# Optimization experiments

Hardware: AMD Instinct MI355X
Metric: run time of the kernel (lower is better)

Reference implementation:

```python
import jax, jax.numpy as jnp
import numpy as np

V, E, H, B, S, T, OOV = 50000, 128, 256, 32, 400, 16, 20


def setup_inputs() -> dict:
    key = jax.random.key(0)
    ks = jax.random.split(key, 20)
    def p(i, shape, s=0.02):
        return jax.random.normal(ks[i], shape, dtype=jnp.float32) * s
    z = lambda *shape: jnp.zeros(shape, dtype=jnp.float32)
    return {
        'input_seq': jax.random.randint(ks[0], (B, S), 0, V),
        'input_seq_ext': jax.random.randint(ks[1], (B, S), 0, V + OOV),
        'target_seq': jax.random.randint(ks[2], (B, T), 0, V),
        'embedding': p(3, (V, E)),
        'enc_Wih_f': p(4, (3 * H, E)), 'enc_Whh_f': p(5, (3 * H, H)),
        'enc_bih_f': z(3 * H), 'enc_bhh_f': z(3 * H),
        'enc_Wih_b': p(6, (3 * H, E)), 'enc_Whh_b': p(7, (3 * H, H)),
        'enc_bih_b': z(3 * H), 'enc_bhh_b': z(3 * H),
        'proj_W': p(8, (H, 2 * H)), 'proj_b': z(H),
        'bridge_W': p(9, (H, 2 * H)), 'bridge_b': z(H),
        'dec_Wih': p(10, (3 * H, E + 2 * H)), 'dec_Whh': p(11, (3 * H, H)),
        'dec_bih': z(3 * H), 'dec_bhh': z(3 * H),
        'attn_Wq': p(12, (H, H)), 'attn_We': p(13, (1, H)),
        'lin_W': p(14, (H, E + 3 * H)), 'lin_b': z(H),
        'pgen_W': p(15, (1, E + 3 * H)), 'pgen_b': z(1),
        'out_W': p(16, (V, H)), 'out_b': z(V),
    }


def gru_cell(x, h, Wih, Whh, bih, bhh):
    # PyTorch GRU cell math
    gi = x @ Wih.T + bih
    gh = h @ Whh.T + bhh
    ir, iz, inn = jnp.split(gi, 3, axis=-1)
    hr, hz, hn = jnp.split(gh, 3, axis=-1)
    r = jax.nn.sigmoid(ir + hr)
    zg = jax.nn.sigmoid(iz + hz)
    n = jnp.tanh(inn + r * hn)
    return (1.0 - zg) * n + zg * h


def run_gru(xs, h0, Wih, Whh, bih, bhh):
    def step(h, x):
        h2 = gru_cell(x, h, Wih, Whh, bih, bhh)
        return h2, h2
    hT, hs = jax.lax.scan(step, h0, xs)
    return hs, hT


def reference(input_seq, input_seq_ext, target_seq, embedding,
              enc_Wih_f, enc_Whh_f, enc_bih_f, enc_bhh_f,
              enc_Wih_b, enc_Whh_b, enc_bih_b, enc_bhh_b,
              proj_W, proj_b, bridge_W, bridge_b,
              dec_Wih, dec_Whh, dec_bih, dec_bhh,
              attn_Wq, attn_We, lin_W, lin_b,
              pgen_W, pgen_b, out_W, out_b):
    Bsz, Slen = input_seq.shape
    Tlen = target_seq.shape[1]
    Hd = bridge_W.shape[0]
    dt = embedding.dtype

    # ---- encoder (bidirectional GRU) ----
    emb_src = embedding[input_seq].transpose(1, 0, 2)  # (S,B,E)
    h0e = jnp.zeros((Bsz, Hd), dt)
    hs_f, hf = run_gru(emb_src, h0e, enc_Wih_f, enc_Whh_f, enc_bih_f, enc_bhh_f)
    hs_b_rev, hb = run_gru(emb_src[::-1], h0e, enc_Wih_b, enc_Whh_b, enc_bih_b, enc_bhh_b)
    enc_states = jnp.concatenate([hs_f, hs_b_rev[::-1]], axis=-1)  # (S,B,2H)
    proj = enc_states @ proj_W.T + proj_b                           # (S,B,H)
    h = jnp.tanh(jnp.concatenate([hf, hb], axis=-1) @ bridge_W.T + bridge_b)  # (B,H)

    rows = jnp.arange(Bsz)
    toks = target_seq[:, :Tlen - 1].T  # teacher forcing, (T-1,B)

    def dec_step(h, tok):
        e = embedding[tok]                                            # (B,E)
        scores = jnp.tanh(h @ attn_Wq.T + proj) @ attn_We[0]          # (S,B)
        alphas = jax.nn.softmax(scores, axis=0)                       # softmax over seq dim
        context = jnp.einsum('sb,sbd->bd', alphas, enc_states)        # (B,2H)
        h2 = gru_cell(jnp.concatenate([e, context], axis=-1), h,
                      dec_Wih, dec_Whh, dec_bih, dec_bhh)             # (B,H)
        cat = jnp.concatenate([e, h2, context], axis=-1)              # (B,E+3H)
        p_gen = jax.nn.sigmoid(cat @ pgen_W.T + pgen_b)               # (B,1)
        logits = (cat @ lin_W.T + lin_b) @ out_W.T + out_b            # (B,V)
        gen = p_gen * jax.nn.softmax(logits, axis=-1)
        attn = (1.0 - p_gen) * alphas.T                               # (B,S)
        ext = jnp.concatenate([gen, jnp.zeros((Bsz, OOV), dt)], axis=-1) + 1e-12
        ext = ext.at[rows[:, None], input_seq_ext].add(attn)          # scatter_add copy dist
        return h2, jnp.log(ext)

    _, outs = jax.lax.scan(dec_step, h, toks)                         # (T-1,B,V+OOV)
    out0 = jnp.zeros((1,) + outs.shape[1:], outs.dtype)               # t=0 row stays zero
    return jnp.concatenate([out0, outs], axis=0)                      # (T,B,V+OOV)
```

## Files before the change

### kernel.cpp

```cpp
#include <hip/hip_runtime.h>

#define SLEN 400
#define BATCH 32
#define TLEN 16
#define NDEC 15
#define EDIM 128
#define HDIM 256
#define H3 768
#define VVOC 50000
#define VEXT 50020
#define SCHUNK 50

__device__ __forceinline__ float frcp(float x){ return __builtin_amdgcn_rcpf(x); }
__device__ __forceinline__ float fsig(float x){ return frcp(1.f + __expf(-x)); }
__device__ __forceinline__ float ftanh(float x){
  float e = __expf(2.f*x);
  return 1.f - 2.f*frcp(e + 1.f);
}

typedef _Float16 h2 __attribute__((ext_vector_type(2)));
typedef _Float16 half8 __attribute__((ext_vector_type(8)));
typedef float floatx4 __attribute__((ext_vector_type(4)));

__device__ __forceinline__ h2 u2h(unsigned u){ return __builtin_bit_cast(h2, u); }
__device__ __forceinline__ unsigned pkh(float a, float b){
  h2 v; v.x=(_Float16)a; v.y=(_Float16)b;
  return __builtin_bit_cast(unsigned, v);
}

#if __has_builtin(__builtin_amdgcn_fdot2)
__device__ __forceinline__ float fdot2h(h2 a, h2 b, float c){
  return __builtin_amdgcn_fdot2(a, b, c, false);
}
#else
__device__ __forceinline__ float fdot2h(h2 a, h2 b, float c){
  return fmaf((float)a.x,(float)b.x, fmaf((float)a.y,(float)b.y, c));
}
#endif

__device__ __forceinline__ float wred_sum(float v){
  #pragma unroll
  for (int o=32;o>0;o>>=1) v += __shfl_down(v,o,64);
  return v;
}
__device__ __forceinline__ float wred_max(float v){
  #pragma unroll
  for (int o=32;o>0;o>>=1) v = fmaxf(v, __shfl_down(v,o,64));
  return v;
}
__device__ __forceinline__ float block_max(float v, float* red){
  v = wred_max(v);
  int lane = threadIdx.x & 63, wid = threadIdx.x >> 6;
  if (!lane) red[wid] = v;
  __syncthreads();
  if (threadIdx.x == 0){
    float m = red[0];
    int nw = blockDim.x >> 6;
    for (int w=1;w<nw;++w) m = fmaxf(m, red[w]);
    red[0] = m;
  }
  __syncthreads();
  v = red[0];
  __syncthreads();
  return v;
}
__device__ __forceinline__ float block_sum(float v, float* red){
  v = wred_sum(v);
  int lane = threadIdx.x & 63, wid = threadIdx.x >> 6;
  if (!lane) red[wid] = v;
  __syncthreads();
  if (threadIdx.x == 0){
    float m = red[0];
    int nw = blockDim.x >> 6;
    for (int w=1;w<nw;++w) m += red[w];
    red[0] = m;
  }
  __syncthreads();
  v = red[0];
  __syncthreads();
  return v;
}

__global__ __launch_bounds__(64) void k_embed(
    const int* __restrict__ input_seq, const int* __restrict__ target_seq,
    const float* __restrict__ embedding,
    _Float16* __restrict__ emb16, float* __restrict__ cat_all, _Float16* __restrict__ cat16)
{
  int row = blockIdx.x;
  if (row < SLEN*BATCH) {
    int s = row >> 5, b = row & 31;
    int tok = input_seq[b*SLEN + s];
    float2 v = ((const float2*)(embedding + (size_t)tok*EDIM))[threadIdx.x];
    ((unsigned*)(emb16 + (size_t)row*EDIM))[threadIdx.x] = pkh(v.x, v.y);
  } else {
    int rr = row - SLEN*BATCH;
    int t = rr >> 5, b = rr & 31;
    int tok = target_seq[b*TLEN + t];
    float2 v = ((const float2*)(embedding + (size_t)tok*EDIM))[threadIdx.x];
    ((float2*)(cat_all + (size_t)rr*896))[threadIdx.x] = v;
    ((unsigned*)(cat16 + (size_t)rr*896))[threadIdx.x] = pkh(v.x, v.y);
  }
}

__global__ __launch_bounds__(256) void k_cvtv(
    const float* __restrict__ S, _Float16* __restrict__ D, int n8)
{
  int i = blockIdx.x*256 + threadIdx.x;
  if (i >= n8) return;
  float4 a = ((const float4*)S)[i*2];
  float4 b = ((const float4*)S)[i*2+1];
  uint4 o;
  o.x = pkh(a.x,a.y); o.y = pkh(a.z,a.w);
  o.z = pkh(b.x,b.y); o.w = pkh(b.z,b.w);
  ((uint4*)D)[i] = o;
}

__global__ void k_cvtk(
    const float* __restrict__ W, uint4* __restrict__ D, int ldw, int coloff)
{
  int row = blockIdx.x, k8 = threadIdx.x, nrows = gridDim.x;
  const float* s = W + (size_t)row*ldw + coloff + k8*8;
  float4 x = *(const float4*)s;
  float4 y = *(const float4*)(s+4);
  uint4 o;
  o.x = pkh(x.x,x.y); o.y = pkh(x.z,x.w);
  o.z = pkh(y.x,y.y); o.w = pkh(y.z,y.w);
  D[(size_t)k8*nrows + row] = o;
}

__global__ __launch_bounds__(256) void k_gmm(
    const _Float16* __restrict__ A, int lda,
    const _Float16* __restrict__ W, int ldw,
    const float* __restrict__ bias,
    float* __restrict__ C, _Float16* __restrict__ C16, int ldc,
    int M, int N, int K, int rev)
{
  __shared__ __align__(16) _Float16 Al[128*64];
  __shared__ __align__(16) _Float16 Wl[128*64];
  int tid = threadIdx.x;
  int wv = tid >> 6, l = tid & 63;
  int wr = (wv>>1)*64, wc = (wv&1)*64;
  int lr = l & 15, lh = l >> 4;
  int m0 = blockIdx.y*128, n0 = blockIdx.x*128;
  floatx4 acc[4][4];
  #pragma unroll
  for (int i=0;i<4;++i)
    #pragma unroll
    for (int jn=0;jn<4;++jn) acc[i][jn] = (floatx4){0.f,0.f,0.f,0.f};

  for (int kc=0; kc<K; kc+=64){
    #pragma unroll
    for (int i=0;i<4;++i){
      int idx = tid + i*256;
      int row = idx>>3, c = idx&7;
      int m = m0+row;
      uint4 v = {0u,0u,0u,0u};
      if (m < M){
        int am = m;
        if (rev){ int s = m>>5; am = ((SLEN-1-s)<<5)|(m&31); }
        v = *(const uint4*)&A[(size_t)am*lda + kc + c*8];
      }
      *(uint4*)&Al[row*64 + ((c ^ (row&7))<<3)] = v;
    }
    #pragma unroll
    for (int i=0;i<4;++i){
      int idx = tid + i*256;
      int row = idx>>3, c = idx&7;
      int n = n0+row;
      uint4 v = {0u,0u,0u,0u};
      if (n < N) v = *(const uint4*)&W[(size_t)n*ldw + kc + c*8];
      *(uint4*)&Wl[row*64 + ((c ^ (row&7))<<3)] = v;
    }
    __syncthreads();
    #pragma unroll
    for (int ks=0; ks<2; ++ks){
      half8 af0, af1, af2, af3, bf0, bf1, bf2, bf3;
      {
        int c = ks*4 + lh;
        int r0 = wr + 0*16 + lr, r1 = wr + 1*16 + lr, r2 = wr + 2*16 + lr, r3 = wr + 3*16 + lr;
        af0 = *(const half8*)&Al[r0*64 + ((c ^ (r0&7))<<3)];
        af1 = *(const half8*)&Al[r1*64 + ((c ^ (r1&7))<<3)];
        af2 = *(const half8*)&Al[r2*64 + ((c ^ (r2&7))<<3)];
        af3 = *(const half8*)&Al[r3*64 + ((c ^ (r3&7))<<3)];
        int n0l = wc + 0*16 + lr, n1l = wc + 1*16 + lr, n2l = wc + 2*16 + lr, n3l = wc + 3*16 + lr;
        bf0 = *(const half8*)&Wl[n0l*64 + ((c ^ (n0l&7))<<3)];
        bf1 = *(const half8*)&Wl[n1l*64 + ((c ^ (n1l&7))<<3)];
        bf2 = *(const half8*)&Wl[n2l*64 + ((c ^ (n2l&7))<<3)];
        bf3 = *(const half8*)&Wl[n3l*64 + ((c ^ (n3l&7))<<3)];
      }
      half8 afs[4] = {af0, af1, af2, af3};
      half8 bfs[4] = {bf0, bf1, bf2, bf3};
      #pragma unroll
      for (int mi=0;mi<4;++mi)
        #pragma unroll
        for (int ni=0;ni<4;++ni)
          acc[mi][ni] = __builtin_amdgcn_mfma_f32_16x16x32_f16(afs[mi], bfs[ni], acc[mi][ni], 0,0,0);
    }
    __syncthreads();
  }
  #pragma unroll
  for (int mi=0;mi<4;++mi){
    #pragma unroll
    for (int q=0;q<4;++q){
      int m = m0 + wr + mi*16 + lh*4 + q;
      if (m < M){
        #pragma unroll
        for (int ni=0;ni<4;++ni){
          int n = n0 + wc + ni*16 + lr;
          if (n < N){
            float v = acc[mi][ni][q] + bias[n];
            if (C)   C[(size_t)m*ldc + n] = v;
            if (C16) C16[(size_t)m*ldc + n] = (_Float16)v;
          }
        }
      }
    }
  }
}

#define L20(M) M(12) M(13) M(14) M(15) M(16) M(17) M(18) M(19) M(20) M(21) \
               M(22) M(23) M(24) M(25) M(26) M(27) M(28) M(29) M(30) M(31)

__global__ __launch_bounds__(768) void k_enc(
    const float* __restrict__ gi_f, const float* __restrict__ gi_b,
    const uint4* __restrict__ W16_f, const uint4* __restrict__ W16_b,
    const float* __restrict__ bhh_f, const float* __restrict__ bhh_b,
    float* __restrict__ enc_states)
{
  int dir = blockIdx.x >> 5, b = blockIdx.x & 31;
  int jj = threadIdx.x;
  const float* gi  = dir ? gi_b  : gi_f;
  const uint4* Wp  = (dir ? W16_b : W16_f) + jj;
  float bh = (dir ? bhh_b : bhh_f)[jj];

  __shared__ __align__(16) unsigned hpk[HDIM/2];
  __shared__ __align__(16) float st[H3];
  __shared__ uint4 Wlds[12][H3];

  #pragma unroll
  for (int k8=0;k8<12;++k8) Wlds[k8][jj] = Wp[k8*H3];

  if (jj < HDIM/2) hpk[jj] = 0u;
  float hreg = 0.f;
  float* dst = enc_states + (size_t)b*2*HDIM + dir*HDIM + jj;
  __syncthreads();

  for (int s=0;s<SLEN;++s){
    const float* grow = gi + ((size_t)s*BATCH + b)*H3;
    float g1 = 0.f, g2 = 0.f;
    if (jj < 512)  g1 = grow[jj];
    if (jj < HDIM) g2 = grow[2*HDIM + jj];
#define DL(i) uint4 p##i = Wp[(i)*H3];
    L20(DL)
#undef DL
    float ac0=0.f, ac1=0.f, ac2=0.f, ac3=0.f;
    #pragma unroll
    for (int k8=0;k8<12;++k8){
      uint4 w = Wlds[k8][jj];
      uint4 hq = *(const uint4*)&hpk[k8*4];
      ac0 = fdot2h(u2h(w.x),u2h(hq.x),ac0);
      ac1 = fdot2h(u2h(w.y),u2h(hq.y),ac1);
      ac2 = fdot2h(u2h(w.z),u2h(hq.z),ac2);
      ac3 = fdot2h(u2h(w.w),u2h(hq.w),ac3);
    }
#define DU(i) { uint4 hq = *(const uint4*)&hpk[(i)*4]; \
    ac0 = fdot2h(u2h(p##i.x),u2h(hq.x),ac0); \
    ac1 = fdot2h(u2h(p##i.y),u2h(hq.y),ac1); \
    ac2 = fdot2h(u2h(p##i.z),u2h(hq.z),ac2); \
    ac3 = fdot2h(u2h(p##i.w),u2h(hq.w),ac3); }
    L20(DU)
#undef DU
    float acc = (ac0+ac1)+(ac2+ac3) + bh;
    st[jj] = (jj < 512) ? (acc + g1) : acc;
    __syncthreads();
    if (jj < HDIM){
      float rr = fsig(st[jj]);
      float zz = fsig(st[HDIM + jj]);
      float nn = ftanh(g2 + rr*st[2*HDIM + jj]);
      float h2v = nn + zz*(hreg - nn);
      hreg = h2v;
      int srow = dir ? (SLEN-1-s) : s;
      dst[(size_t)srow*BATCH*2*HDIM] = h2v;
      ((_Float16*)hpk)[jj] = (_Float16)h2v;
    }
    __syncthreads();
  }
}

__global__ __launch_bounds__(256) void k_bridge(
    const float* __restrict__ enc_states,
    const float* __restrict__ bridge_W, const float* __restrict__ bridge_b,
    float* __restrict__ h_out)
{
  int b = blockIdx.x, j = threadIdx.x;
  __shared__ float hcat[2*HDIM];
  hcat[j]        = enc_states[((size_t)(SLEN-1)*BATCH + b)*2*HDIM + j];
  hcat[HDIM + j] = enc_states[(size_t)b*2*HDIM + HDIM + j];
  __syncthreads();
  const float* w = bridge_W + (size_t)j*2*HDIM;
  float4 a = {0.f,0.f,0.f,0.f};
  #pragma unroll 4
  for (int k=0;k<2*HDIM;k+=4){
    float4 h4 = *(const float4*)&hcat[k];
    float4 w4 = *(const float4*)&w[k];
    a.x=fmaf(h4.x,w4.x,a.x); a.y=fmaf(h4.y,w4.y,a.y);
    a.z=fmaf(h4.z,w4.z,a.z); a.w=fmaf(h4.w,w4.w,a.w);
  }
  h_out[b*HDIM+j] = ftanh((a.x+a.y)+(a.z+a.w) + bridge_b[j]);
}

__global__ __launch_bounds__(256) void k_attnB(
    int t,
    const _Float16* __restrict__ proj16,
    const _Float16* __restrict__ enc16,
    const uint4* __restrict__ Wq16k,
    const float* __restrict__ attn_We,
    const float* __restrict__ hin,
    float* __restrict__ alphas_e,
    float* __restrict__ sum_part,
    float* __restrict__ ctx_part)
{
  int ch = blockIdx.x, b = blockIdx.y;
  int tid = threadIdx.x;
  __shared__ float q_s[HDIM], we_s[HDIM], sc[SCHUNK], red[8];
  __shared__ __align__(16) unsigned hq[HDIM/2];

  we_s[tid] = attn_We[tid];
  if (tid < HDIM/2){
    float2 hv = *(const float2*)&hin[b*HDIM + tid*2];
    hq[tid] = pkh(hv.x, hv.y);
  }
  __syncthreads();
  {
    float a0=0.f,a1=0.f,a2=0.f,a3=0.f;
    #pragma unroll
    for (int k8=0;k8<32;++k8){
      uint4 w = Wq16k[(size_t)k8*HDIM + tid];
      uint4 hp = *(const uint4*)&hq[k8*4];
      a0 = fdot2h(u2h(w.x),u2h(hp.x),a0);
      a1 = fdot2h(u2h(w.y),u2h(hp.y),a1);
      a2 = fdot2h(u2h(w.z),u2h(hp.z),a2);
      a3 = fdot2h(u2h(w.w),u2h(hp.w),a3);
    }
    q_s[tid] = (a0+a1)+(a2+a3);
  }
  __syncthreads();
  {
    int wave = tid >> 6, lane = tid & 63;
    int d0 = lane*4;
    float4 qv = *(const float4*)&q_s[d0];
    float4 wv = *(const float4*)&we_s[d0];
    for (int is = wave; is < SCHUNK; is += 4){
      int s = ch*SCHUNK + is;
      uint2 p = *(const uint2*)&proj16[((size_t)(s*BATCH + b))*HDIM + d0];
      h2 pa = u2h(p.x), pb = u2h(p.y);
      float v = ftanh(qv.x+(float)pa.x)*wv.x + ftanh(qv.y+(float)pa.y)*wv.y
              + ftanh(qv.z+(float)pb.x)*wv.z + ftanh(qv.w+(float)pb.y)*wv.w;
      v = wred_sum(v);
      if (lane == 0){
        float e = __expf(v);
        sc[is] = e;
        alphas_e[((size_t)t*SLEN + s)*BATCH + b] = e;
      }
    }
  }
  __syncthreads();
  {
    float sv = (tid < SCHUNK) ? sc[tid] : 0.f;
    sv = block_sum(sv, red);
    if (tid == 0) sum_part[b*8 + ch] = sv;
  }
  {
    float a0=0.f, a1=0.f;
    for (int is=0; is<SCHUNK; ++is){
      int s = ch*SCHUNK + is;
      unsigned u = *(const unsigned*)&enc16[((size_t)(s*BATCH + b) << 9) + tid*2];
      h2 ev = u2h(u);
      float e = sc[is];
      a0 = fmaf(e, (float)ev.x, a0);
      a1 = fmaf(e, (float)ev.y, a1);
    }
    float2 o; o.x = a0; o.y = a1;
    *(float2*)&ctx_part[(((size_t)b*8 + ch) << 9) + tid*2] = o;
  }
}

__global__ __launch_bounds__(256) void k_gruD(
    int t,
    const float* __restrict__ ctx_part,
    const float* __restrict__ sum_part,
    const float* __restrict__ gie_all,
    const uint4* __restrict__ dWck16,
    const uint4* __restrict__ dWhk16,
    const float* __restrict__ dec_bhh,
    const float* __restrict__ hin,
    float* __restrict__ hout,
    float* __restrict__ cat_all, _Float16* __restrict__ cat16,
    float* __restrict__ sums_all)
{
  int ch = blockIdx.x, b = blockIdx.y;
  int tid = threadIdx.x;
  int jl = tid & 31, slice = tid >> 5;
  __shared__ __align__(16) unsigned cpk[HDIM], hpk[HDIM/2];
  __shared__ float hf[HDIM];
  __shared__ float pc[3][8][32], ph[3][8][32];
  __shared__ float invs;

  if (tid == 0){
    float ssum = 0.f;
    #pragma unroll
    for (int c=0;c<8;++c) ssum += sum_part[b*8 + c];
    float inv = 1.f/ssum;
    invs = inv;
    if (ch == 0) sums_all[t*BATCH + b] = inv;
  }
  if (tid < HDIM/2){
    float2 hv = *(const float2*)&hin[b*HDIM + tid*2];
    hpk[tid] = pkh(hv.x, hv.y);
    hf[tid*2] = hv.x; hf[tid*2+1] = hv.y;
  }
  __syncthreads();
  {
    int d0 = tid*2;
    float c0=0.f, c1=0.f;
    #pragma unroll
    for (int c=0;c<8;++c){
      float2 v = *(const float2*)&ctx_part[(((size_t)b*8 + c) << 9) + d0];
      c0 += v.x; c1 += v.y;
    }
    c0 *= invs; c1 *= invs;
    cpk[tid] = pkh(c0, c1);
    if (ch == 0){
      int r = t*BATCH + b;
      cat_all[(size_t)r*896 + 384 + d0]     = c0;
      cat_all[(size_t)r*896 + 384 + d0 + 1] = c1;
      cat16[(size_t)r*896 + 384 + d0]     = (_Float16)c0;
      cat16[(size_t)r*896 + 384 + d0 + 1] = (_Float16)c1;
    }
  }
  __syncthreads();
  {
    int jb = ch*32 + jl;
    float c0=0.f,c1=0.f,c2=0.f, g0=0.f,g1=0.f,g2=0.f;
    #pragma unroll
    for (int i=0;i<8;++i){
      int k8 = slice*8 + i;
      uint4 hq = *(const uint4*)&cpk[k8*4];
      uint4 w0 = dWck16[(size_t)k8*H3 + jb];
      uint4 w1 = dWck16[(size_t)k8*H3 + 256 + jb];
      uint4 w2 = dWck16[(size_t)k8*H3 + 512 + jb];
      c0 = fdot2h(u2h(w0.x),u2h(hq.x),c0); c0 = fdot2h(u2h(w0.y),u2h(hq.y),c0);
      c0 = fdot2h(u2h(w0.z),u2h(hq.z),c0); c0 = fdot2h(u2h(w0.w),u2h(hq.w),c0);
      c1 = fdot2h(u2h(w1.x),u2h(hq.x),c1); c1 = fdot2h(u2h(w1.y),u2h(hq.y),c1);
      c1 = fdot2h(u2h(w1.z),u2h(hq.z),c1); c1 = fdot2h(u2h(w1.w),u2h(hq.w),c1);
      c2 = fdot2h(u2h(w2.x),u2h(hq.x),c2); c2 = fdot2h(u2h(w2.y),u2h(hq.y),c2);
      c2 = fdot2h(u2h(w2.z),u2h(hq.z),c2); c2 = fdot2h(u2h(w2.w),u2h(hq.w),c2);
    }
    #pragma unroll
    for (int i=0;i<4;++i){
      int k8 = slice*4 + i;
      uint4 hq = *(const uint4*)&hpk[k8*4];
      uint4 w0 = dWhk16[(size_t)k8*H3 + jb];
      uint4 w1 = dWhk16[(size_t)k8*H3 + 256 + jb];
      uint4 w2 = dWhk16[(size_t)k8*H3 + 512 + jb];
      g0 = fdot2h(u2h(w0.x),u2h(hq.x),g0); g0 = fdot2h(u2h(w0.y),u2h(hq.y),g0);
      g0 = fdot2h(u2h(w0.z),u2h(hq.z),g0); g0 = fdot2h(u2h(w0.w),u2h(hq.w),g0);
      g1 = fdot2h(u2h(w1.x),u2h(hq.x),g1); g1 = fdot2h(u2h(w1.y),u2h(hq.y),g1);
      g1 = fdot2h(u2h(w1.z),u2h(hq.z),g1); g1 = fdot2h(u2h(w1.w),u2h(hq.w),g1);
      g2 = fdot2h(u2h(w2.x),u2h(hq.x),g2); g2 = fdot2h(u2h(w2.y),u2h(hq.y),g2);
      g2 = fdot2h(u2h(w2.z),u2h(hq.z),g2); g2 = fdot2h(u2h(w2.w),u2h(hq.w),g2);
    }
    pc[0][slice][jl]=c0; pc[1][slice][jl]=c1; pc[2][slice][jl]=c2;
    ph[0][slice][jl]=g0; ph[1][slice][jl]=g1; ph[2][slice][jl]=g2;
  }
  __syncthreads();
  if (tid < 32){
    int j = tid, r = t*BATCH + b;
    int jj = ch*32 + j;
    float gi0 = gie_all[(size_t)r*H3 + jj];
    float gi1 = gie_all[(size_t)r*H3 + 256 + jj];
    float gi2 = gie_all[(size_t)r*H3 + 512 + jj];
    float gh0 = dec_bhh[jj], gh1 = dec_bhh[256 + jj], gh2 = dec_bhh[512 + jj];
    #pragma unroll
    for (int c=0;c<8;++c){
      gi0 += pc[0][c][j]; gi1 += pc[1][c][j]; gi2 += pc[2][c][j];
      gh0 += ph[0][c][j]; gh1 += ph[1][c][j]; gh2 += ph[2][c][j];
    }
    float rr = fsig(gi0 + gh0);
    float zz = fsig(gi1 + gh1);
    float nn = ftanh(gi2 + rr*gh2);
    float hp = hf[jj];
    float h2v = nn + zz*(hp - nn);
    hout[b*HDIM + jj] = h2v;
    cat_all[(size_t)r*896 + 128 + jj] = h2v;
    cat16[(size_t)r*896 + 128 + jj] = (_Float16)h2v;
  }
}

__global__ __launch_bounds__(64) void k_pgen(
    const float* __restrict__ cat_all,
    const float* __restrict__ pgen_W, const float* __restrict__ pgen_b,
    float* __restrict__ pgen_all)
{
  int r = blockIdx.x;
  const float* c = cat_all + (size_t)r*896;
  float acc = 0.f;
  for (int k=threadIdx.x; k<896; k+=64) acc = fmaf(c[k], pgen_W[k], acc);
  acc = wred_sum(acc);
  if (threadIdx.x==0) pgen_all[r] = fsig(acc + pgen_b[0]);
}

__global__ __launch_bounds__(256) void k_rowred(
    const _Float16* __restrict__ logits,
    float* __restrict__ row_max, float* __restrict__ row_sum)
{
  int r = blockIdx.x;
  const uint4* row = (const uint4*)(logits + (size_t)r*VVOC);
  __shared__ float red[8];
  float m = -1e30f;
  for (int v=threadIdx.x; v<VVOC/8; v+=256){
    uint4 x = row[v];
    h2 a=u2h(x.x), bb=u2h(x.y), c=u2h(x.z), d=u2h(x.w);
    float m1 = fmaxf(fmaxf((float)a.x,(float)a.y), fmaxf((float)bb.x,(float)bb.y));
    float m2 = fmaxf(fmaxf((float)c.x,(float)c.y), fmaxf((float)d.x,(float)d.y));
    m = fmaxf(m, fmaxf(m1,m2));
  }
  m = block_max(m, red);
  float s = 0.f;
  for (int v=threadIdx.x; v<VVOC/8; v+=256){
    uint4 x = row[v];
    h2 a=u2h(x.x), bb=u2h(x.y), c=u2h(x.z), d=u2h(x.w);
    s += __expf((float)a.x-m) + __expf((float)a.y-m) + __expf((float)bb.x-m) + __expf((float)bb.y-m)
       + __expf((float)c.x-m) + __expf((float)c.y-m) + __expf((float)d.x-m) + __expf((float)d.y-m);
  }
  s = block_sum(s, red);
  if (threadIdx.x==0){ row_max[r]=m; row_sum[r]=1.f/s; }
}

__global__ __launch_bounds__(256) void k_final(
    const _Float16* __restrict__ logits, const float* __restrict__ pgen_all,
    const float* __restrict__ row_max, const float* __restrict__ row_sum,
    float* __restrict__ out)
{
  int v = blockIdx.x*256 + threadIdx.x;
  if (v >= VEXT) return;
  int b = blockIdx.y, t = blockIdx.z;
  size_t o = ((size_t)t*BATCH + b)*VEXT + v;
  if (t == 0){ out[o] = 0.f; return; }
  int r = (t-1)*BATCH + b;
  float val = 1e-12f;
  if (v < VVOC)
    val += pgen_all[r] * row_sum[r] * __expf((float)logits[(size_t)r*VVOC + v] - row_max[r]);
  out[o] = val;
}

__global__ __launch_bounds__(512) void k_scatter(
    const int* __restrict__ input_seq_ext,
    const float* __restrict__ alphas_e, const float* __restrict__ sums_all,
    const float* __restrict__ pgen_all,
    float* __restrict__ out)
{
  int r = blockIdx.x;
  int s = threadIdx.x;
  if (s >= SLEN) return;
  int t = r >> 5, b = r & 31;
  float w = (1.f - pgen_all[r]) * alphas_e[((size_t)t*SLEN + s)*BATCH + b] * sums_all[r];
  int idx = input_seq_ext[b*SLEN + s];
  atomicAdd(&out[((size_t)(t+1)*BATCH + b)*VEXT + idx], w);
}

__global__ __launch_bounds__(256) void k_log(float* __restrict__ out)
{
  int v = blockIdx.x*256 + threadIdx.x;
  if (v >= VEXT) return;
  int b = blockIdx.y, t = blockIdx.z + 1;
  size_t o = ((size_t)t*BATCH + b)*VEXT + v;
  out[o] = __logf(out[o]);
}

extern "C" void kernel_launch(void* const* d_in, const int* in_sizes, int n_in,
                              void* d_out, int out_size, void* d_ws, size_t ws_size,
                              hipStream_t stream)
{
  (void)in_sizes; (void)n_in; (void)out_size; (void)ws_size;
  const int*   input_seq     = (const int*)d_in[0];
  const int*   input_seq_ext = (const int*)d_in[1];
  const int*   target_seq    = (const int*)d_in[2];
  const float* embedding     = (const float*)d_in[3];
  const float* enc_Wih_f     = (const float*)d_in[4];
  const float* enc_Whh_f     = (const float*)d_in[5];
  const float* enc_bih_f     = (const float*)d_in[6];
  const float* enc_bhh_f     = (const float*)d_in[7];
  const float* enc_Wih_b     = (const float*)d_in[8];
  const float* enc_Whh_b     = (const float*)d_in[9];
  const float* enc_bih_b     = (const float*)d_in[10];
  const float* enc_bhh_b     = (const float*)d_in[11];
  const float* proj_W        = (const float*)d_in[12];
  const float* proj_b        = (const float*)d_in[13];
  const float* bridge_W      = (const float*)d_in[14];
  const float* bridge_b      = (const float*)d_in[15];
  const float* dec_Wih       = (const float*)d_in[16];
  const float* dec_Whh       = (const float*)d_in[17];
  const float* dec_bih       = (const float*)d_in[18];
  const float* dec_bhh       = (const float*)d_in[19];
  const float* attn_Wq       = (const float*)d_in[20];
  const float* attn_We       = (const float*)d_in[21];
  const float* lin_W         = (const float*)d_in[22];
  const float* lin_b         = (const float*)d_in[23];
  const float* pgen_W        = (const float*)d_in[24];
  const float* pgen_b        = (const float*)d_in[25];
  const float* out_W         = (const float*)d_in[26];
  const float* out_b         = (const float*)d_in[27];
  float* out = (float*)d_out;
  float* ws  = (float*)d_ws;

  _Float16* emb16    = (_Float16*)(ws + 0);
  _Float16* Wih16_f  = (_Float16*)(ws + 409600);
  _Float16* Wih16_b  = (_Float16*)(ws + 458752);
  _Float16* proj_W16 = (_Float16*)(ws + 507904);
  _Float16* lin_W16  = (_Float16*)(ws + 573440);
  _Float16* cat16    = (_Float16*)(ws + 688128);
  _Float16* lin16    = (_Float16*)(ws + 903168);
  _Float16* dWih16   = (_Float16*)(ws + 964608);
  float* enc_states  = ws + 1638400;
  _Float16* proj16   = (_Float16*)(ws + 8192000);
  float* gi_f        = ws + 11468800;
  float* gi_b        = ws + 21299200;
  _Float16* logits16 = (_Float16*)(ws + 11468800);
  _Float16* out_W16  = (_Float16*)(ws + 23468800);
  _Float16* enc16    = (_Float16*)(ws + 29868800);
  uint4* Wq16k       = (uint4*)(ws + 33145600);
  uint4* dWck16      = (uint4*)(ws + 33178368);
  uint4* dWhk16      = (uint4*)(ws + 33374976);
  float* ctx_part    = ws + 33473280;
  float* sum_part    = ws + 33604352;
  float* sums_all    = ws + 33604608;
  float* hbuf0       = ws + 33605088;
  float* hbuf1       = ws + 33613280;
  uint4* W16_f       = (uint4*)(ws + 35000000);
  uint4* W16_b       = (uint4*)(ws + 35098304);
  float* cat_all     = ws + 35468800;
  float* gie_all     = ws + 35898880;
  float* alphas_e    = ws + 36275712;
  float* pgen_all    = ws + 36467712;
  float* row_max     = ws + 36468192;
  float* row_sum     = ws + 36468672;

  k_embed<<<dim3(SLEN*BATCH + NDEC*BATCH), dim3(64), 0, stream>>>(
      input_seq, target_seq, embedding, emb16, cat_all, cat16);

  k_cvtv<<<dim3((98304/8+255)/256), dim3(256), 0, stream>>>(enc_Wih_f, Wih16_f, 98304/8);
  k_cvtv<<<dim3((98304/8+255)/256), dim3(256), 0, stream>>>(enc_Wih_b, Wih16_b, 98304/8);
  k_cvtv<<<dim3((131072/8+255)/256), dim3(256), 0, stream>>>(proj_W, proj_W16, 131072/8);
  k_cvtv<<<dim3((229376/8+255)/256), dim3(256), 0, stream>>>(lin_W, lin_W16, 229376/8);
  k_cvtv<<<dim3((491520/8+255)/256), dim3(256), 0, stream>>>(dec_Wih, dWih16, 491520/8);
  k_cvtk<<<dim3(H3), dim3(32), 0, stream>>>(enc_Whh_f, W16_f, HDIM, 0);
  k_cvtk<<<dim3(H3), dim3(32), 0, stream>>>(enc_Whh_b, W16_b, HDIM, 0);
  k_cvtk<<<dim3(H3), dim3(64), 0, stream>>>(dec_Wih, dWck16, 640, 128);
  k_cvtk<<<dim3(H3), dim3(32), 0, stream>>>(dec_Whh, dWhk16, HDIM, 0);
  k_cvtk<<<dim3(HDIM), dim3(32), 0, stream>>>(attn_Wq, Wq16k, HDIM, 0);

  k_gmm<<<dim3(6,100), dim3(256), 0, stream>>>(emb16, EDIM, Wih16_f, EDIM, enc_bih_f,
      gi_f, (_Float16*)nullptr, H3, SLEN*BATCH, H3, EDIM, 0);
  k_gmm<<<dim3(6,100), dim3(256), 0, stream>>>(emb16, EDIM, Wih16_b, EDIM, enc_bih_b,
      gi_b, (_Float16*)nullptr, H3, SLEN*BATCH, H3, EDIM, 1);

  k_enc<<<dim3(64), dim3(768), 0, stream>>>(gi_f, gi_b, W16_f, W16_b, enc_bhh_f, enc_bhh_b, enc_states);

  k_cvtv<<<dim3((6553600/8+255)/256), dim3(256), 0, stream>>>(enc_states, enc16, 6553600/8);
  k_cvtv<<<dim3((12800000/8+255)/256), dim3(256), 0, stream>>>(out_W, out_W16, 12800000/8);

  k_gmm<<<dim3(2,100), dim3(256), 0, stream>>>(enc16, 2*HDIM, proj_W16, 2*HDIM, proj_b,
      (float*)nullptr, proj16, HDIM, SLEN*BATCH, HDIM, 2*HDIM, 0);

  k_bridge<<<dim3(BATCH), dim3(256), 0, stream>>>(enc_states, bridge_W, bridge_b, hbuf0);

  k_gmm<<<dim3(6,4), dim3(256), 0, stream>>>(cat16, 896, dWih16, 640, dec_bih,
      gie_all, (_Float16*)nullptr, H3, NDEC*BATCH, H3, EDIM, 0);

  float* hb[2] = {hbuf0, hbuf1};
  for (int t=0;t<NDEC;++t){
    k_attnB<<<dim3(8,32), dim3(256), 0, stream>>>(t, proj16, enc16, Wq16k, attn_We,
        hb[t&1], alphas_e, sum_part, ctx_part);
    k_gruD<<<dim3(8,32), dim3(256), 0, stream>>>(t, ctx_part, sum_part, gie_all,
        dWck16, dWhk16, dec_bhh, hb[t&1], hb[(t+1)&1], cat_all, cat16, sums_all);
  }

  k_gmm<<<dim3(2,4), dim3(256), 0, stream>>>(cat16, 896, lin_W16, 896, lin_b,
      (float*)nullptr, lin16, HDIM, NDEC*BATCH, HDIM, 896, 0);
  k_pgen<<<dim3(NDEC*BATCH), dim3(64), 0, stream>>>(cat_all, pgen_W, pgen_b, pgen_all);
  k_gmm<<<dim3(391,4), dim3(256), 0, stream>>>(lin16, HDIM, out_W16, HDIM, out_b,
      (float*)nullptr, logits16, VVOC, NDEC*BATCH, VVOC, HDIM, 0);
  k_rowred<<<dim3(NDEC*BATCH), dim3(256), 0, stream>>>(logits16, row_max, row_sum);
  k_final<<<dim3(196, BATCH, TLEN), dim3(256), 0, stream>>>(logits16, pgen_all, row_max, row_sum, out);
  k_scatter<<<dim3(NDEC*BATCH), dim3(512), 0, stream>>>(input_seq_ext, alphas_e, sums_all, pgen_all, out);
  k_log<<<dim3(196, BATCH, NDEC), dim3(256), 0, stream>>>(out);
}
```

Measured before the change: 1.198 ms.

## Batch weight conversions, hoist encoder weight loads, write fp16 encoder states directly

Merges the five vector and five transposing weight-conversion launches into two batched launches indexed by blockIdx.y. The encoder now loads its 20 non-LDS weight chunks into registers once before the time loop instead of reloading them every step. It also writes fp16 encoder states directly and saves the final hidden states for the bridge, removing the fp32 enc_states buffer and its separate conversion pass. The trade-off is heavier register pressure in the 768-thread encoder block, which could force spills.

```diff
diff --git a/kernel.cpp b/kernel.cpp
--- a/kernel.cpp
+++ b/kernel.cpp
@@ -102,9 +102,21 @@
   }
 }
 
-__global__ __launch_bounds__(256) void k_cvtv(
-    const float* __restrict__ S, _Float16* __restrict__ D, int n8)
-{
+__global__ __launch_bounds__(256) void k_cvtv5(
+    const float* __restrict__ S0, _Float16* __restrict__ D0, int n0,
+    const float* __restrict__ S1, _Float16* __restrict__ D1, int n1,
+    const float* __restrict__ S2, _Float16* __restrict__ D2, int n2,
+    const float* __restrict__ S3, _Float16* __restrict__ D3, int n3,
+    const float* __restrict__ S4, _Float16* __restrict__ D4, int n4)
+{
+  const float* S; _Float16* D; int n8;
+  switch (blockIdx.y){
+    case 0: S=S0; D=D0; n8=n0; break;
+    case 1: S=S1; D=D1; n8=n1; break;
+    case 2: S=S2; D=D2; n8=n2; break;
+    case 3: S=S3; D=D3; n8=n3; break;
+    default: S=S4; D=D4; n8=n4; break;
+  }
   int i = blockIdx.x*256 + threadIdx.x;
   if (i >= n8) return;
   float4 a = ((const float4*)S)[i*2];
@@ -115,10 +127,36 @@
   ((uint4*)D)[i] = o;
 }
 
-__global__ void k_cvtk(
-    const float* __restrict__ W, uint4* __restrict__ D, int ldw, int coloff)
-{
-  int row = blockIdx.x, k8 = threadIdx.x, nrows = gridDim.x;
+__global__ __launch_bounds__(256) void k_cvtv(
+    const float* __restrict__ S, _Float16* __restrict__ D, int n8)
+{
+  int i = blockIdx.x*256 + threadIdx.x;
+  if (i >= n8) return;
+  float4 a = ((const float4*)S)[i*2];
+  float4 b = ((const float4*)S)[i*2+1];
+  uint4 o;
+  o.x = pkh(a.x,a.y); o.y = pkh(a.z,a.w);
+  o.z = pkh(b.x,b.y); o.w = pkh(b.z,b.w);
+  ((uint4*)D)[i] = o;
+}
+
+__global__ __launch_bounds__(64) void k_cvtk5(
+    const float* __restrict__ W0, uint4* __restrict__ D0,
+    const float* __restrict__ W1, uint4* __restrict__ D1,
+    const float* __restrict__ W2, uint4* __restrict__ D2,
+    const float* __restrict__ W3, uint4* __restrict__ D3,
+    const float* __restrict__ W4, uint4* __restrict__ D4)
+{
+  const float* W; uint4* D; int ldw, coloff, nrows, nk8;
+  switch (blockIdx.y){
+    case 0: W=W0; D=D0; ldw=HDIM; coloff=0;   nrows=H3;   nk8=32; break;
+    case 1: W=W1; D=D1; ldw=HDIM; coloff=0;   nrows=H3;   nk8=32; break;
+    case 2: W=W2; D=D2; ldw=640;  coloff=128; nrows=H3;   nk8=64; break;
+    case 3: W=W3; D=D3; ldw=HDIM; coloff=0;   nrows=H3;   nk8=32; break;
+    default: W=W4; D=D4; ldw=HDIM; coloff=0;  nrows=HDIM; nk8=32; break;
+  }
+  int row = blockIdx.x, k8 = threadIdx.x;
+  if (row >= nrows || k8 >= nk8) return;
   const float* s = W + (size_t)row*ldw + coloff + k8*8;
   float4 x = *(const float4*)s;
   float4 y = *(const float4*)(s+4);
@@ -218,14 +256,14 @@
   }
 }
 
-#define L20(M) M(12) M(13) M(14) M(15) M(16) M(17) M(18) M(19) M(20) M(21) \
-               M(22) M(23) M(24) M(25) M(26) M(27) M(28) M(29) M(30) M(31)
+#define R20(M) M(0) M(1) M(2) M(3) M(4) M(5) M(6) M(7) M(8) M(9) \
+               M(10) M(11) M(12) M(13) M(14) M(15) M(16) M(17) M(18) M(19)
 
 __global__ __launch_bounds__(768) void k_enc(
     const float* __restrict__ gi_f, const float* __restrict__ gi_b,
     const uint4* __restrict__ W16_f, const uint4* __restrict__ W16_b,
     const float* __restrict__ bhh_f, const float* __restrict__ bhh_b,
-    float* __restrict__ enc_states)
+    _Float16* __restrict__ enc16, float* __restrict__ hfin)
 {
   int dir = blockIdx.x >> 5, b = blockIdx.x & 31;
   int jj = threadIdx.x;
@@ -240,9 +278,13 @@
   #pragma unroll
   for (int k8=0;k8<12;++k8) Wlds[k8][jj] = Wp[k8*H3];
 
+#define DW(i) uint4 q##i = Wp[(12+(i))*H3];
+  R20(DW)
+#undef DW
+
   if (jj < HDIM/2) hpk[jj] = 0u;
   float hreg = 0.f;
-  float* dst = enc_states + (size_t)b*2*HDIM + dir*HDIM + jj;
+  _Float16* dst = enc16 + (size_t)b*2*HDIM + dir*HDIM + jj;
   __syncthreads();
 
   for (int s=0;s<SLEN;++s){
@@ -250,9 +292,6 @@
     float g1 = 0.f, g2 = 0.f;
     if (jj < 512)  g1 = grow[jj];
     if (jj < HDIM) g2 = grow[2*HDIM + jj];
-#define DL(i) uint4 p##i = Wp[(i)*H3];
-    L20(DL)
-#undef DL
     float ac0=0.f, ac1=0.f, ac2=0.f, ac3=0.f;
     #pragma unroll
     for (int k8=0;k8<12;++k8){
@@ -263,12 +302,12 @@
       ac2 = fdot2h(u2h(w.z),u2h(hq.z),ac2);
       ac3 = fdot2h(u2h(w.w),u2h(hq.w),ac3);
     }
-#define DU(i) { uint4 hq = *(const uint4*)&hpk[(i)*4]; \
-    ac0 = fdot2h(u2h(p##i.x),u2h(hq.x),ac0); \
-    ac1 = fdot2h(u2h(p##i.y),u2h(hq.y),ac1); \
-    ac2 = fdot2h(u2h(p##i.z),u2h(hq.z),ac2); \
-    ac3 = fdot2h(u2h(p##i.w),u2h(hq.w),ac3); }
-    L20(DU)
+#define DU(i) { uint4 hq = *(const uint4*)&hpk[(12+(i))*4]; \
+    ac0 = fdot2h(u2h(q##i.x),u2h(hq.x),ac0); \
+    ac1 = fdot2h(u2h(q##i.y),u2h(hq.y),ac1); \
+    ac2 = fdot2h(u2h(q##i.z),u2h(hq.z),ac2); \
+    ac3 = fdot2h(u2h(q##i.w),u2h(hq.w),ac3); }
+    R20(DU)
 #undef DU
     float acc = (ac0+ac1)+(ac2+ac3) + bh;
     st[jj] = (jj < 512) ? (acc + g1) : acc;
@@ -280,22 +319,23 @@
       float h2v = nn + zz*(hreg - nn);
       hreg = h2v;
       int srow = dir ? (SLEN-1-s) : s;
-      dst[(size_t)srow*BATCH*2*HDIM] = h2v;
+      dst[(size_t)srow*BATCH*2*HDIM] = (_Float16)h2v;
       ((_Float16*)hpk)[jj] = (_Float16)h2v;
+      if (s == SLEN-1) hfin[(size_t)(dir*BATCH + b)*HDIM + jj] = h2v;
     }
     __syncthreads();
   }
 }
 
 __global__ __launch_bounds__(256) void k_bridge(
-    const float* __restrict__ enc_states,
+    const float* __restrict__ hfin,
     const float* __restrict__ bridge_W, const float* __restrict__ bridge_b,
     float* __restrict__ h_out)
 {
   int b = blockIdx.x, j = threadIdx.x;
   __shared__ float hcat[2*HDIM];
-  hcat[j]        = enc_states[((size_t)(SLEN-1)*BATCH + b)*2*HDIM + j];
-  hcat[HDIM + j] = enc_states[(size_t)b*2*HDIM + HDIM + j];
+  hcat[j]        = hfin[(size_t)b*HDIM + j];
+  hcat[HDIM + j] = hfin[(size_t)(BATCH + b)*HDIM + j];
   __syncthreads();
   const float* w = bridge_W + (size_t)j*2*HDIM;
   float4 a = {0.f,0.f,0.f,0.f};
@@ -622,13 +662,13 @@
   _Float16* cat16    = (_Float16*)(ws + 688128);
   _Float16* lin16    = (_Float16*)(ws + 903168);
   _Float16* dWih16   = (_Float16*)(ws + 964608);
-  float* enc_states  = ws + 1638400;
+  _Float16* enc16    = (_Float16*)(ws + 1638400);
+  float* hfin        = ws + 4915200;
   _Float16* proj16   = (_Float16*)(ws + 8192000);
   float* gi_f        = ws + 11468800;
   float* gi_b        = ws + 21299200;
   _Float16* logits16 = (_Float16*)(ws + 11468800);
   _Float16* out_W16  = (_Float16*)(ws + 23468800);
-  _Float16* enc16    = (_Float16*)(ws + 29868800);
   uint4* Wq16k       = (uint4*)(ws + 33145600);
   uint4* dWck16      = (uint4*)(ws + 33178368);
   uint4* dWhk16      = (uint4*)(ws + 33374976);
@@ -649,31 +689,33 @@
   k_embed<<<dim3(SLEN*BATCH + NDEC*BATCH), dim3(64), 0, stream>>>(
       input_seq, target_seq, embedding, emb16, cat_all, cat16);
 
-  k_cvtv<<<dim3((98304/8+255)/256), dim3(256), 0, stream>>>(enc_Wih_f, Wih16_f, 98304/8);
-  k_cvtv<<<dim3((98304/8+255)/256), dim3(256), 0, stream>>>(enc_Wih_b, Wih16_b, 98304/8);
-  k_cvtv<<<dim3((131072/8+255)/256), dim3(256), 0, stream>>>(proj_W, proj_W16, 131072/8);
-  k_cvtv<<<dim3((229376/8+255)/256), dim3(256), 0, stream>>>(lin_W, lin_W16, 229376/8);
-  k_cvtv<<<dim3((491520/8+255)/256), dim3(256), 0, stream>>>(dec_Wih, dWih16, 491520/8);
-  k_cvtk<<<dim3(H3), dim3(32), 0, stream>>>(enc_Whh_f, W16_f, HDIM, 0);
-  k_cvtk<<<dim3(H3), dim3(32), 0, stream>>>(enc_Whh_b, W16_b, HDIM, 0);
-  k_cvtk<<<dim3(H3), dim3(64), 0, stream>>>(dec_Wih, dWck16, 640, 128);
-  k_cvtk<<<dim3(H3), dim3(32), 0, stream>>>(dec_Whh, dWhk16, HDIM, 0);
-  k_cvtk<<<dim3(HDIM), dim3(32), 0, stream>>>(attn_Wq, Wq16k, HDIM, 0);
+  k_cvtv5<<<dim3(240, 5), dim3(256), 0, stream>>>(
+      enc_Wih_f, Wih16_f, 12288,
+      enc_Wih_b, Wih16_b, 12288,
+      proj_W,    proj_W16, 16384,
+      lin_W,     lin_W16,  28672,
+      dec_Wih,   dWih16,   61440);
+  k_cvtk5<<<dim3(H3, 5), dim3(64), 0, stream>>>(
+      enc_Whh_f, W16_f,
+      enc_Whh_b, W16_b,
+      dec_Wih,   dWck16,
+      dec_Whh,   dWhk16,
+      attn_Wq,   Wq16k);
 
   k_gmm<<<dim3(6,100), dim3(256), 0, stream>>>(emb16, EDIM, Wih16_f, EDIM, enc_bih_f,
       gi_f, (_Float16*)nullptr, H3, SLEN*BATCH, H3, EDIM, 0);
   k_gmm<<<dim3(6,100), dim3(256), 0, stream>>>(emb16, EDIM, Wih16_b, EDIM, enc_bih_b,
       gi_b, (_Float16*)nullptr, H3, SLEN*BATCH, H3, EDIM, 1);
 
-  k_enc<<<dim3(64), dim3(768), 0, stream>>>(gi_f, gi_b, W16_f, W16_b, enc_bhh_f, enc_bhh_b, enc_states);
-
-  k_cvtv<<<dim3((6553600/8+255)/256), dim3(256), 0, stream>>>(enc_states, enc16, 6553600/8);
+  k_enc<<<dim3(64), dim3(768), 0, stream>>>(gi_f, gi_b, W16_f, W16_b, enc_bhh_f, enc_bhh_b,
+      enc16, hfin);
+
   k_cvtv<<<dim3((12800000/8+255)/256), dim3(256), 0, stream>>>(out_W, out_W16, 12800000/8);
 
   k_gmm<<<dim3(2,100), dim3(256), 0, stream>>>(enc16, 2*HDIM, proj_W16, 2*HDIM, proj_b,
       (float*)nullptr, proj16, HDIM, SLEN*BATCH, HDIM, 2*HDIM, 0);
 
-  k_bridge<<<dim3(BATCH), dim3(256), 0, stream>>>(enc_states, bridge_W, bridge_b, hbuf0);
+  k_bridge<<<dim3(BATCH), dim3(256), 0, stream>>>(hfin, bridge_W, bridge_b, hbuf0);
 
   k_gmm<<<dim3(6,4), dim3(256), 0, stream>>>(cat16, 896, dWih16, 640, dec_bih,
       gie_all, (_Float16*)nullptr, H3, NDEC*BATCH, H3, EDIM, 0);
```

Result: no change. 1.176 ms (-1.8%).
